# Optimization experiments

Measured on AMD Instinct MI355X. Metric: run time of the kernel, lower is better.

The kernel has to match this reference:

```python
import jax, jax.numpy as jnp
import numpy as np

B, CIN, CINT, H, W = 2, 2048, 512, 96, 96
CQK = CINT // 8  # 64, mmcv CrissCrossAttention query/key channels
NG = 32          # GroupNorm groups
EPS = 1e-5


def conv1x1(x, w, b):
    # x: [B,C,H,W], w: [O,C,1,1], b: [O]
    y = jnp.einsum('bchw,oc->bohw', x, w[:, :, 0, 0])
    return y + b[None, :, None, None]


def conv3x3(x, w):
    return jax.lax.conv_general_dilated(
        x, w, window_strides=(1, 1), padding=((1, 1), (1, 1)),
        dimension_numbers=('NCHW', 'OIHW', 'NCHW'))


def group_norm(x, gamma, beta):
    b, c, h, w = x.shape
    xg = x.reshape(b, NG, c // NG, h, w)
    mu = xg.mean(axis=(2, 3, 4), keepdims=True)
    var = xg.var(axis=(2, 3, 4), keepdims=True)
    xg = (xg - mu) * jax.lax.rsqrt(var + EPS)
    return xg.reshape(b, c, h, w) * gamma[None, :, None, None] + beta[None, :, None, None]


def criss_cross_attention(x, qw, qb, kw, kb, vw, vb, gamma):
    # mmcv CrissCrossAttention: attention restricted to each pixel's row + column.
    b, c, h, w = x.shape
    q = conv1x1(x, qw, qb)  # [B,Cqk,H,W]
    k = conv1x1(x, kw, kb)  # [B,Cqk,H,W]
    v = conv1x1(x, vw, vb)  # [B,C,H,W]
    # column (H-direction) energy: e_H[b,h,w,i] = sum_c q[b,c,h,w] k[b,c,i,w]
    e_h = jnp.einsum('bchw,bciw->bhwi', q, k)
    diag = jnp.eye(h, dtype=bool)[:, None, :]  # mask i==h (self counted once, in W branch)
    e_h = jnp.where(diag, -jnp.inf, e_h)
    # row (W-direction) energy: e_W[b,h,w,j] = sum_c q[b,c,h,w] k[b,c,h,j]
    e_w = jnp.einsum('bchw,bchj->bhwj', q, k)
    attn = jax.nn.softmax(jnp.concatenate([e_h, e_w], axis=-1), axis=-1)  # [B,H,W,H+W]
    a_h, a_w = attn[..., :h], attn[..., h:]
    out = jnp.einsum('bciw,bhwi->bchw', v, a_h) + jnp.einsum('bchj,bhwj->bchw', v, a_w)
    return gamma * out + x


def setup_inputs() -> dict:
    key = jax.random.key(0)
    ks = jax.random.split(key, 12)
    s = 0.02
    return {
        'x': jax.random.normal(ks[0], (B, CIN, H, W), jnp.float32),
        'conv1_w': jax.random.normal(ks[1], (CINT, CIN, 1, 1), jnp.float32) * s,
        'conv1_b': jnp.zeros((CINT,), jnp.float32),
        'q_w': jax.random.normal(ks[2], (CQK, CINT, 1, 1), jnp.float32) * s,
        'q_b': jnp.zeros((CQK,), jnp.float32),
        'k_w': jax.random.normal(ks[3], (CQK, CINT, 1, 1), jnp.float32) * s,
        'k_b': jnp.zeros((CQK,), jnp.float32),
        'v_w': jax.random.normal(ks[4], (CINT, CINT, 1, 1), jnp.float32) * s,
        'v_b': jnp.zeros((CINT,), jnp.float32),
        'gamma': jnp.asarray(0.5, jnp.float32),
        'convout_w': jax.random.normal(ks[5], (CINT, CINT, 3, 3), jnp.float32) * s,
        'gn_gamma': jnp.ones((CINT,), jnp.float32),
        'gn_beta': jnp.zeros((CINT,), jnp.float32),
    }


def reference(x, conv1_w, conv1_b, q_w, q_b, k_w, k_b, v_w, v_b, gamma,
              convout_w, gn_gamma, gn_beta):
    out = conv1x1(x, conv1_w, conv1_b)
    for _ in range(2):  # recurrence = 2
        out = criss_cross_attention(out, q_w, q_b, k_w, k_b, v_w, v_b, gamma)
    out = conv3x3(out, convout_w)  # ConvModule with GN => conv has no bias
    out = group_norm(out, gn_gamma, gn_beta)
    return out
```

## Files before the change

kernel.cpp:

```cpp
#include <hip/hip_runtime.h>
#include <hip/hip_bf16.h>


typedef __bf16 bf8_t __attribute__((ext_vector_type(8)));
typedef float f32x4 __attribute__((ext_vector_type(4)));

union I4B8 { int4 i; bf8_t b; };

typedef const __attribute__((address_space(1))) void as1_cvoid;
typedef __attribute__((address_space(3))) void as3_void;
__device__ __forceinline__ void gload16(const void* g, void* l) {
  __builtin_amdgcn_global_load_lds((as1_cvoid*)g, (as3_void*)l, 16, 0, 0);
}
__device__ __forceinline__ int rot8(int c, int key) { return (c + key) & 7; }

__global__ __launch_bounds__(256) void cast_rot_k(const float* s, __bf16* d, int K8, int total8) {
  int idx = blockIdx.x * 256 + threadIdx.x;
  if (idx >= total8) return;
  int c8 = idx % K8, n = idx / K8;
  int cch = c8 & 7;
  int pos = rot8(cch, n & 7);
  const float* sp = s + ((long long)n * K8 + c8) * 8;
  float4 a = *(const float4*)sp, b = *(const float4*)(sp + 4);
  I4B8 u;
  u.b[0] = (__bf16)a.x; u.b[1] = (__bf16)a.y; u.b[2] = (__bf16)a.z; u.b[3] = (__bf16)a.w;
  u.b[4] = (__bf16)b.x; u.b[5] = (__bf16)b.y; u.b[6] = (__bf16)b.z; u.b[7] = (__bf16)b.w;
  *(int4*)(d + ((long long)n * K8 + (c8 & ~7) + pos) * 8) = u.i;
}

__global__ __launch_bounds__(256) void wqkv_rot_k(const float* qw, const float* kw, const float* vw, __bf16* d) {
  int idx = blockIdx.x * 256 + threadIdx.x;
  if (idx >= 640 * 64) return;
  int c8 = idx & 63, n = idx >> 6;
  const float* src = (n < 64) ? qw + (long long)n * 512
                   : (n < 128) ? kw + (long long)(n - 64) * 512
                               : vw + (long long)(n - 128) * 512;
  int cch = c8 & 7;
  int pos = rot8(cch, n & 7);
  const float* sp = src + c8 * 8;
  float4 a = *(const float4*)sp, b = *(const float4*)(sp + 4);
  I4B8 u;
  u.b[0] = (__bf16)a.x; u.b[1] = (__bf16)a.y; u.b[2] = (__bf16)a.z; u.b[3] = (__bf16)a.w;
  u.b[4] = (__bf16)b.x; u.b[5] = (__bf16)b.y; u.b[6] = (__bf16)b.z; u.b[7] = (__bf16)b.w;
  *(int4*)(d + ((long long)n * 64 + (c8 & ~7) + pos) * 8) = u.i;
}

__global__ __launch_bounds__(256) void fuse_bias_k(const float* qb, const float* kb, const float* vb, float* d) {
  int i = blockIdx.x * 256 + threadIdx.x;
  if (i >= 640) return;
  d[i] = (i < 64) ? qb[i] : (i < 128) ? kb[i - 64] : vb[i - 128];
}

__global__ __launch_bounds__(256) void reorder_w_k(const float* w, __bf16* wr) {
  int idx = blockIdx.x * 256 + threadIdx.x;
  if (idx >= 512 * 9 * 64) return;
  int ch8 = idx & 63;
  int r = idx >> 6;
  int dydx = r % 9, o = r / 9;
  int k = dydx * 512 + ch8 * 8;
  int cch = (k >> 3) & 7;
  int pos = rot8(cch, o & 7);
  const float* src = w + ((long long)o * 512 + ch8 * 8) * 9 + dydx;
  I4B8 u;
#pragma unroll
  for (int j = 0; j < 8; j++) u.b[j] = (__bf16)src[j * 9];
  *(int4*)(wr + (long long)o * 4608 + (k & ~63) + pos * 8) = u.i;
}

__global__ __launch_bounds__(256) void transpose_x_k(const float* x, __bf16* xt) {
  __shared__ __bf16 l[64 * 66];
  int c0 = blockIdx.x * 64, s0 = blockIdx.y * 64, b = blockIdx.z;
  int t = threadIdx.x;
#pragma unroll
  for (int i = 0; i < 2; i++) {
    int slot = t + i * 256;
    int cl = slot >> 3, sch = slot & 7;
    const float* src = x + ((long long)(b * 2048 + c0 + cl)) * 9216 + s0 + sch * 8;
    float4 a = *(const float4*)src, bb = *(const float4*)(src + 4);
    __bf16* dst = &l[cl * 66 + sch * 8];
    dst[0] = (__bf16)a.x; dst[1] = (__bf16)a.y; dst[2] = (__bf16)a.z; dst[3] = (__bf16)a.w;
    dst[4] = (__bf16)bb.x; dst[5] = (__bf16)bb.y; dst[6] = (__bf16)bb.z; dst[7] = (__bf16)bb.w;
  }
  __syncthreads();
#pragma unroll
  for (int i = 0; i < 2; i++) {
    int slot = t + i * 256;
    int sl = slot >> 3, cch = slot & 7;
    I4B8 u;
#pragma unroll
    for (int j = 0; j < 8; j++) u.b[j] = l[(cch * 8 + j) * 66 + sl];
    *(int4*)(xt + ((long long)(b * 9216 + s0 + sl)) * 2048 + c0 + rot8(cch, sl & 7) * 8) = u.i;
  }
}

__global__ __launch_bounds__(256) void pad_k(const __bf16* y, __bf16* pout) {
  long long idx = (long long)blockIdx.x * 256 + threadIdx.x;
  int cch = (int)(idx & 63);
  long long r = idx >> 6;
  int ww = (int)(r % 98);
  long long r2 = r / 98;
  int hh = (int)(r2 % 98);
  int b = (int)(r2 / 98);
  int slice = cch >> 3, sub = cch & 7;
  int4 v = make_int4(0, 0, 0, 0);
  if (hh >= 1 && hh <= 96 && ww >= 1 && ww <= 96) {
    long long pix = (long long)b * 9216 + (hh - 1) * 96 + (ww - 1);
    v = *(const int4*)(y + pix * 512 + (slice * 8 + rot8(sub, (int)(pix & 7))) * 8);
  }
  *(int4*)(pout + r * 512 + (slice * 8 + rot8(sub, ww & 7)) * 8) = v;
}

struct GemmAP {
  const __bf16 *A, *B;
  __bf16* C;
  const float* bias;
  long long sAr, sBr, sCr;
  int K, ntn;
};

template <int CROT>
__global__ __launch_bounds__(256) void gemm_async_k(GemmAP p) {
  __shared__ __attribute__((aligned(16))) __bf16 lA[128 * 64];
  __shared__ __attribute__((aligned(16))) __bf16 lB[128 * 64];
  const int t = threadIdx.x;
  const int id = blockIdx.x;
  const int per8 = gridDim.x >> 3;
  const int lin = (id & 7) * per8 + (id >> 3);
  const int m0 = (lin / p.ntn) * 128, n0 = (lin % p.ntn) * 128;
  const int lane = t & 63, wave = t >> 6;
  const int wm = (wave >> 1) * 64, wn = (wave & 1) * 64;
  const int l15 = lane & 15, l4 = lane >> 4;
  const int srow = (lane >> 3), schunk = (lane & 7) * 8;
  f32x4 acc[4][4];
#pragma unroll
  for (int i = 0; i < 4; i++)
#pragma unroll
    for (int j = 0; j < 4; j++) acc[i][j] = f32x4{0.f, 0.f, 0.f, 0.f};

  for (int kb = 0; kb < p.K; kb += 64) {
    const int rb = wave * 32;
#pragma unroll
    for (int i = 0; i < 4; i++) {
      int row = rb + i * 8;
      gload16(p.A + (long long)(m0 + row + srow) * p.sAr + kb + schunk, &lA[row * 64]);
      gload16(p.B + (long long)(n0 + row + srow) * p.sBr + kb + schunk, &lB[row * 64]);
    }
    __syncthreads();
#pragma unroll
    for (int kk = 0; kk < 2; kk++) {
      bf8_t af[4], bfr[4];
      int cch = kk * 4 + l4;
#pragma unroll
      for (int mt = 0; mt < 4; mt++) {
        int r = wm + mt * 16 + l15;
        af[mt] = *(bf8_t*)&lA[r * 64 + (rot8(cch, r & 7) << 3)];
      }
#pragma unroll
      for (int nt = 0; nt < 4; nt++) {
        int r = wn + nt * 16 + l15;
        bfr[nt] = *(bf8_t*)&lB[r * 64 + (rot8(cch, r & 7) << 3)];
      }
#pragma unroll
      for (int mt = 0; mt < 4; mt++)
#pragma unroll
        for (int nt = 0; nt < 4; nt++)
          acc[mt][nt] = __builtin_amdgcn_mfma_f32_16x16x32_bf16(af[mt], bfr[nt], acc[mt][nt], 0, 0, 0);
    }
    __syncthreads();
  }
#pragma unroll
  for (int nt = 0; nt < 4; nt++) {
    int col = n0 + wn + nt * 16 + l15;
    float bv = p.bias[col];
#pragma unroll
    for (int mt = 0; mt < 4; mt++) {
      int row0 = m0 + wm + mt * 16 + (l4 << 2);
#pragma unroll
      for (int r = 0; r < 4; r++) {
        int row = row0 + r;
        int pc = CROT ? (col & ~63) + (rot8((col >> 3) & 7, row & 7) << 3) + (col & 7) : col;
        p.C[(long long)row * p.sCr + pc] = (__bf16)(acc[mt][nt][r] + bv);
      }
    }
  }
}

struct GemmP {
  const __bf16 *A, *B;
  __bf16* C;
  long long sAr, sAb1, sAb2;
  long long sBr, sBb1, sBb2;
  long long sCr, sCb1, sCb2;
  int M, N, K, bdiv, mode;
  const __bf16 *tmp, *res;
  const float* gma;
};

template <int CROT>
__global__ __launch_bounds__(256) void gemm_bt_k(GemmP p) {
  __shared__ __attribute__((aligned(16))) __bf16 lA[128 * 64];
  __shared__ __attribute__((aligned(16))) __bf16 lB[128 * 64];
  const int t = threadIdx.x;
  const int z = blockIdx.z;
  const int z1 = z / p.bdiv, z2 = z % p.bdiv;
  const __bf16* A = p.A + (long long)z1 * p.sAb1 + (long long)z2 * p.sAb2;
  const __bf16* B = p.B + (long long)z1 * p.sBb1 + (long long)z2 * p.sBb2;
  const int m0 = blockIdx.y * 128, n0 = blockIdx.x * 128;
  const int lane = t & 63, wave = t >> 6;
  const int wm = (wave >> 1) * 64, wn = (wave & 1) * 64;
  const int l15 = lane & 15, l4 = lane >> 4;
  f32x4 acc[4][4];
#pragma unroll
  for (int i = 0; i < 4; i++)
#pragma unroll
    for (int j = 0; j < 4; j++) acc[i][j] = f32x4{0.f, 0.f, 0.f, 0.f};

  int arow[4];
#pragma unroll
  for (int i = 0; i < 4; i++) {
    int slot = t + i * 256;
    arow[i] = min(m0 + (slot >> 3), p.M - 1);
  }
  for (int kb = 0; kb < p.K; kb += 64) {
#pragma unroll
    for (int i = 0; i < 4; i++) {
      int slot = t + i * 256;
      int r = slot >> 3, c = slot & 7;
      int gk = kb + c * 8;
      int4 v = make_int4(0, 0, 0, 0);
      if (gk < p.K) v = *(const int4*)(A + (long long)arow[i] * p.sAr + gk);
      *(int4*)&lA[r * 64 + (rot8(c, r & 7) << 3)] = v;
    }
#pragma unroll
    for (int i = 0; i < 4; i++) {
      int slot = t + i * 256;
      int kl = slot & 63, cch = slot >> 6;
      int gk = kb + kl;
      I4B8 u;
      u.i = make_int4(0, 0, 0, 0);
      if (gk < p.K) u.i = *(const int4*)(B + (long long)gk * p.sBr + n0 + cch * 8);
#pragma unroll
      for (int j = 0; j < 8; j++) {
        int n = cch * 8 + j;
        lB[n * 64 + (rot8(kl >> 3, n & 7) << 3) + (kl & 7)] = u.b[j];
      }
    }
    __syncthreads();
#pragma unroll
    for (int kk = 0; kk < 2; kk++) {
      bf8_t af[4], bfr[4];
      int cch = kk * 4 + l4;
#pragma unroll
      for (int mt = 0; mt < 4; mt++) {
        int r = wm + mt * 16 + l15;
        af[mt] = *(bf8_t*)&lA[r * 64 + (rot8(cch, r & 7) << 3)];
      }
#pragma unroll
      for (int nt = 0; nt < 4; nt++) {
        int r = wn + nt * 16 + l15;
        bfr[nt] = *(bf8_t*)&lB[r * 64 + (rot8(cch, r & 7) << 3)];
      }
#pragma unroll
      for (int mt = 0; mt < 4; mt++)
#pragma unroll
        for (int nt = 0; nt < 4; nt++)
          acc[mt][nt] = __builtin_amdgcn_mfma_f32_16x16x32_bf16(af[mt], bfr[nt], acc[mt][nt], 0, 0, 0);
    }
    __syncthreads();
  }
  long long coff = (long long)z1 * p.sCb1 + (long long)z2 * p.sCb2;
  float g = (p.mode == 2) ? *p.gma : 0.f;
#pragma unroll
  for (int nt = 0; nt < 4; nt++) {
    int col = n0 + wn + nt * 16 + l15;
    if (col >= p.N) continue;
#pragma unroll
    for (int mt = 0; mt < 4; mt++) {
      int row0 = m0 + wm + mt * 16 + (l4 << 2);
#pragma unroll
      for (int r = 0; r < 4; r++) {
        int row = row0 + r;
        if (row >= p.M) continue;
        long long offL = coff + (long long)row * p.sCr + col;
        long long offP = offL;
        if (CROT)
          offP = coff + (long long)row * p.sCr +
                 (col & ~63) + (rot8((col >> 3) & 7, row & 7) << 3) + (col & 7);
        float v = acc[mt][nt][r];
        if (p.mode == 2)
          v = g * ((float)p.tmp[offL] + v) + (float)p.res[offP];
        p.C[offP] = (__bf16)v;
      }
    }
  }
}

__global__ __launch_bounds__(384) void cc_scores_k(const __bf16* qkv, float* attnf) {
  __shared__ __attribute__((aligned(16))) __bf16 Qs[96 * 64];
  __shared__ __attribute__((aligned(16))) __bf16 Ks[96 * 64];
  int bfi = blockIdx.x;
  int b = bfi / 96, f = bfi % 96;
  int mode = blockIdx.y;
  long long base = (mode == 0) ? ((long long)(b * 9216 + f)) * 640 : ((long long)(b * 9216 + f * 96)) * 640;
  long long rstr = (mode == 0) ? 96 * 640 : 640;
  int t = threadIdx.x;
#pragma unroll
  for (int i = 0; i < 2; i++) {
    int slot = t + i * 384;
    int r = slot >> 3, c = slot & 7;
    int sw = rot8(c, r & 7) << 3;
    *(int4*)&Qs[r * 64 + sw] = *(const int4*)(qkv + base + (long long)r * rstr + c * 8);
    *(int4*)&Ks[r * 64 + sw] = *(const int4*)(qkv + base + (long long)r * rstr + 64 + c * 8);
  }
  __syncthreads();
  int lane = t & 63, wave = t >> 6;
  int l15 = lane & 15, l4 = lane >> 4;
  f32x4 acc[6];
#pragma unroll
  for (int i = 0; i < 6; i++) acc[i] = f32x4{0.f, 0.f, 0.f, 0.f};
#pragma unroll
  for (int kk = 0; kk < 2; kk++) {
    int ar = wave * 16 + l15;
    int cch = kk * 4 + l4;
    bf8_t af = *(bf8_t*)&Qs[ar * 64 + (rot8(cch, ar & 7) << 3)];
#pragma unroll
    for (int nt = 0; nt < 6; nt++) {
      int br = nt * 16 + l15;
      bf8_t bfr = *(bf8_t*)&Ks[br * 64 + (rot8(cch, br & 7) << 3)];
      acc[nt] = __builtin_amdgcn_mfma_f32_16x16x32_bf16(af, bfr, acc[nt], 0, 0, 0);
    }
  }
#pragma unroll
  for (int nt = 0; nt < 6; nt++) {
#pragma unroll
    for (int r = 0; r < 4; r++) {
      int m = wave * 16 + (l4 << 2) + r;
      int n = nt * 16 + l15;
      float v = acc[nt][r];
      long long off;
      if (mode == 0) {
        if (n == m) v = -__builtin_inff();
        off = ((long long)((b * 96 + m) * 96 + f)) * 192 + n;
      } else {
        off = ((long long)((b * 96 + f) * 96 + m)) * 192 + 96 + n;
      }
      attnf[off] = v;
    }
  }
}

__global__ __launch_bounds__(256) void cc_softmax_k(const float* attnf, __bf16* attnb) {
  int wave = threadIdx.x >> 6, lane = threadIdx.x & 63;
  long long row = (long long)blockIdx.x * 4 + wave;
  const float* src = attnf + row * 192;
  float e0 = src[lane], e1 = src[lane + 64], e2 = src[lane + 128];
  float m = fmaxf(e0, fmaxf(e1, e2));
#pragma unroll
  for (int o = 32; o; o >>= 1) m = fmaxf(m, __shfl_xor(m, o));
  e0 = __expf(e0 - m);
  e1 = __expf(e1 - m);
  e2 = __expf(e2 - m);
  float s = e0 + e1 + e2;
#pragma unroll
  for (int o = 32; o; o >>= 1) s += __shfl_xor(s, o);
  float inv = 1.f / s;
  __bf16* dst = attnb + row * 192;
  dst[lane] = (__bf16)(e0 * inv);
  dst[lane + 64] = (__bf16)(e1 * inv);
  dst[lane + 128] = (__bf16)(e2 * inv);
}

__global__ __launch_bounds__(256) void conv3_gemm_k(const __bf16* pin, const __bf16* wr, __bf16* C) {
  __shared__ __attribute__((aligned(16))) __bf16 lA[128 * 64];
  __shared__ __attribute__((aligned(16))) __bf16 lB[128 * 64];
  const int t = threadIdx.x;
  const int id = blockIdx.x;
  const int per8 = gridDim.x >> 3;
  const int lin = (id & 7) * per8 + (id >> 3);
  const int m0 = (lin >> 2) * 128, n0 = (lin & 3) * 128;
  const int lane = t & 63, wave = t >> 6;
  const int wm = (wave >> 1) * 64, wn = (wave & 1) * 64;
  const int l15 = lane & 15, l4 = lane >> 4;
  const int srow = lane >> 3, schunk = (lane & 7) * 8;
  const int rb = wave * 32;
  f32x4 acc[4][4];
#pragma unroll
  for (int i = 0; i < 4; i++)
#pragma unroll
    for (int j = 0; j < 4; j++) acc[i][j] = f32x4{0.f, 0.f, 0.f, 0.f};
  long long sbase[4], bbase[4];
#pragma unroll
  for (int i = 0; i < 4; i++) {
    int r = rb + i * 8 + srow;
    int m = m0 + r;
    int b = m / 9216, hw = m % 9216;
    int h = hw / 96, w2 = hw % 96;
    sbase[i] = ((long long)b * 9604 + h * 98 + w2) * 512 + schunk;
    bbase[i] = (long long)(n0 + r) * 4608 + schunk;
  }
  int w2f[4];
#pragma unroll
  for (int mt = 0; mt < 4; mt++) w2f[mt] = (m0 + wm + mt * 16 + l15) % 96;

  int kt = 0;
  for (int tap = 0; tap < 9; tap++) {
    const int dy = tap / 3, dx = tap - dy * 3;
    const long long aoff = (long long)(dy * 98 + dx) * 512;
    int keyA[4];
#pragma unroll
    for (int mt = 0; mt < 4; mt++) keyA[mt] = (w2f[mt] + dx) & 7;
    for (int sl = 0; sl < 8; sl++, kt++) {
      const int c0k = sl * 64;
#pragma unroll
      for (int i = 0; i < 4; i++) {
        gload16(pin + sbase[i] + aoff + c0k, &lA[(rb + i * 8) * 64]);
        gload16(wr + bbase[i] + kt * 64, &lB[(rb + i * 8) * 64]);
      }
      __syncthreads();
#pragma unroll
      for (int kk = 0; kk < 2; kk++) {
        bf8_t af[4], bfr[4];
        int cch = kk * 4 + l4;
#pragma unroll
        for (int mt = 0; mt < 4; mt++) {
          int r = wm + mt * 16 + l15;
          af[mt] = *(bf8_t*)&lA[r * 64 + (rot8(cch, keyA[mt]) << 3)];
        }
#pragma unroll
        for (int nt = 0; nt < 4; nt++) {
          int r = wn + nt * 16 + l15;
          bfr[nt] = *(bf8_t*)&lB[r * 64 + (rot8(cch, r & 7) << 3)];
        }
#pragma unroll
        for (int mt = 0; mt < 4; mt++)
#pragma unroll
          for (int nt = 0; nt < 4; nt++)
            acc[mt][nt] = __builtin_amdgcn_mfma_f32_16x16x32_bf16(af[mt], bfr[nt], acc[mt][nt], 0, 0, 0);
      }
      __syncthreads();
    }
  }
#pragma unroll
  for (int nt = 0; nt < 4; nt++) {
    int col = n0 + wn + nt * 16 + l15;
#pragma unroll
    for (int mt = 0; mt < 4; mt++) {
      int row0 = m0 + wm + mt * 16 + (l4 << 2);
#pragma unroll
      for (int r = 0; r < 4; r++) {
        int row = row0 + r;
        C[(long long)row * 512 + col] = (__bf16)acc[mt][nt][r];
      }
    }
  }
}

__global__ __launch_bounds__(256) void gn_stats_k(const __bf16* z, float* stats) {
  int bg = blockIdx.x;
  int b = bg >> 5, g = bg & 31;
  int t = threadIdx.x;
  int cch = t & 1, sp0 = t >> 1;
  const __bf16* base = z + (long long)b * 9216 * 512 + g * 16 + cch * 8;
  float s = 0.f, ss = 0.f;
  for (int sp = sp0; sp < 9216; sp += 128) {
    I4B8 u;
    u.i = *(const int4*)(base + (long long)sp * 512);
#pragma unroll
    for (int j = 0; j < 8; j++) {
      float f = (float)u.b[j];
      s += f;
      ss += f * f;
    }
  }
#pragma unroll
  for (int o = 32; o; o >>= 1) {
    s += __shfl_xor(s, o);
    ss += __shfl_xor(ss, o);
  }
  __shared__ float red[8];
  int wave = t >> 6, lane = t & 63;
  if (lane == 0) {
    red[wave] = s;
    red[4 + wave] = ss;
  }
  __syncthreads();
  if (t == 0) {
    float S = red[0] + red[1] + red[2] + red[3];
    float SS = red[4] + red[5] + red[6] + red[7];
    const float inv = 1.f / 147456.f;
    float mean = S * inv;
    float var = SS * inv - mean * mean;
    stats[2 * bg] = mean;
    stats[2 * bg + 1] = rsqrtf(var + 1e-5f);
  }
}

__global__ __launch_bounds__(256) void gn_write_k(const __bf16* z, const float* stats,
                                                 const float* gng, const float* gnb, float* out) {
  __shared__ __bf16 l[64 * 98];
  int c0 = blockIdx.x * 64, h = blockIdx.y, b = blockIdx.z;
  int t = threadIdx.x;
#pragma unroll
  for (int i = 0; i < 3; i++) {
    int slot = t + i * 256;
    int wl = slot >> 3, cch = slot & 7;
    I4B8 u;
    u.i = *(const int4*)(z + ((long long)(b * 9216 + h * 96 + wl)) * 512 + c0 + cch * 8);
#pragma unroll
    for (int j = 0; j < 8; j++) l[(cch * 8 + j) * 98 + wl] = u.b[j];
  }
  __syncthreads();
#pragma unroll
  for (int i = 0; i < 3; i++) {
    int slot = t + i * 256;
    int wch = slot % 12, cl = slot / 12;
    int c = c0 + cl;
    int g = c >> 4;
    float mean = stats[2 * (b * 32 + g)], rstd = stats[2 * (b * 32 + g) + 1];
    float sc = rstd * gng[c];
    float sh = gnb[c] - mean * sc;
    float4 o0, o1;
    const __bf16* src = &l[cl * 98 + wch * 8];
    o0.x = (float)src[0] * sc + sh; o0.y = (float)src[1] * sc + sh;
    o0.z = (float)src[2] * sc + sh; o0.w = (float)src[3] * sc + sh;
    o1.x = (float)src[4] * sc + sh; o1.y = (float)src[5] * sc + sh;
    o1.z = (float)src[6] * sc + sh; o1.w = (float)src[7] * sc + sh;
    float* dst = out + ((long long)((b * 512 + c) * 96 + h)) * 96 + wch * 8;
    *(float4*)dst = o0;
    *(float4*)(dst + 4) = o1;
  }
}

extern "C" void kernel_launch(void* const* d_in, const int* in_sizes, int n_in,
                              void* d_out, int out_size, void* d_ws, size_t ws_size,
                              hipStream_t stream) {
  (void)in_sizes; (void)n_in; (void)out_size;
  const float* x = (const float*)d_in[0];
  const float* conv1w = (const float*)d_in[1];
  const float* conv1b = (const float*)d_in[2];
  const float* qw = (const float*)d_in[3];
  const float* qbias = (const float*)d_in[4];
  const float* kw = (const float*)d_in[5];
  const float* kbias = (const float*)d_in[6];
  const float* vw = (const float*)d_in[7];
  const float* vbias = (const float*)d_in[8];
  const float* gma = (const float*)d_in[9];
  const float* cow = (const float*)d_in[10];
  const float* gng = (const float*)d_in[11];
  const float* gnb = (const float*)d_in[12];
  float* out = (float*)d_out;

  if (ws_size < 134876160ULL) return;

  char* w = (char*)d_ws;
  __bf16* xt    = (__bf16*)(w);
  __bf16* qkv   = (__bf16*)(w);
  __bf16* attnb = (__bf16*)(w + 23592960);
  __bf16* padb  = (__bf16*)(w);
  __bf16* zb    = (__bf16*)(w + 19668992);
  __bf16* wrot  = (__bf16*)(w + 38543360);
  __bf16* ya    = (__bf16*)(w + 75497472);
  __bf16* yb    = (__bf16*)(w + 94371840);
  __bf16* tmp1  = (__bf16*)(w + 113246208);
  float* attnf  = (float*)(w + 113246208);
  __bf16* c1wb  = (__bf16*)(w + 132120576);
  __bf16* wqkvb = (__bf16*)(w + 134217728);
  float* qkvbias = (float*)(w + 134873088);
  float* stats   = (float*)(w + 134875648);

  cast_rot_k<<<512, 256, 0, stream>>>(conv1w, c1wb, 256, 131072);
  wqkv_rot_k<<<160, 256, 0, stream>>>(qw, kw, vw, wqkvb);
  fuse_bias_k<<<3, 256, 0, stream>>>(qbias, kbias, vbias, qkvbias);
  transpose_x_k<<<dim3(32, 144, 2), 256, 0, stream>>>(x, xt);

  {
    GemmAP p{};
    p.A = xt; p.B = c1wb; p.C = ya; p.bias = conv1b;
    p.sAr = 2048; p.sBr = 2048; p.sCr = 512;
    p.K = 2048; p.ntn = 4;
    gemm_async_k<1><<<576, 256, 0, stream>>>(p);
  }

  for (int it = 0; it < 2; it++) {
    __bf16* tin = it ? yb : ya;
    __bf16* tout = it ? ya : yb;
    {
      GemmAP p{};
      p.A = tin; p.B = wqkvb; p.C = qkv; p.bias = qkvbias;
      p.sAr = 512; p.sBr = 512; p.sCr = 640;
      p.K = 512; p.ntn = 5;
      gemm_async_k<0><<<720, 256, 0, stream>>>(p);
    }
    cc_scores_k<<<dim3(192, 2), 384, 0, stream>>>(qkv, attnf);
    cc_softmax_k<<<4608, 256, 0, stream>>>(attnf, attnb);
    {
      GemmP p{};
      p.A = attnb; p.sAr = 96 * 192; p.sAb1 = (long long)96 * 96 * 192; p.sAb2 = 192;
      p.B = qkv + 128; p.sBr = (long long)96 * 640; p.sBb1 = (long long)9216 * 640; p.sBb2 = 640;
      p.C = tmp1; p.sCr = (long long)96 * 512; p.sCb1 = (long long)9216 * 512; p.sCb2 = 512;
      p.M = 96; p.N = 512; p.K = 96; p.bdiv = 96; p.mode = 0;
      gemm_bt_k<0><<<dim3(4, 1, 192), 256, 0, stream>>>(p);
    }
    {
      GemmP p{};
      p.A = attnb + 96; p.sAr = 192; p.sAb1 = (long long)96 * 96 * 192; p.sAb2 = (long long)96 * 192;
      p.B = qkv + 128; p.sBr = 640; p.sBb1 = (long long)9216 * 640; p.sBb2 = (long long)96 * 640;
      p.C = tout; p.sCr = 512; p.sCb1 = (long long)9216 * 512; p.sCb2 = (long long)96 * 512;
      p.M = 96; p.N = 512; p.K = 96; p.bdiv = 96; p.mode = 2;
      p.tmp = tmp1; p.res = tin; p.gma = gma;
      gemm_bt_k<1><<<dim3(4, 1, 192), 256, 0, stream>>>(p);
    }
  }

  reorder_w_k<<<1152, 256, 0, stream>>>(cow, wrot);
  pad_k<<<4802, 256, 0, stream>>>(ya, padb);
  conv3_gemm_k<<<576, 256, 0, stream>>>(padb, wrot, zb);
  gn_stats_k<<<64, 256, 0, stream>>>(zb, stats);
  gn_write_k<<<dim3(8, 96, 2), 256, 0, stream>>>(zb, stats, gng, gnb, out);
}
```

Before: 693.1 us.

## Split attention buffers, fuse padding into aggregation epilogue, async-load attention tiles

Scores are written in contiguous per-column and per-row blocks, and softmax emits separate swizzled, K-padded H and W attention matrices. The aggregation GEMMs can then load A tiles with async global-to-LDS loads and a fixed K of 128. The final aggregation writes straight into the padded conv input, so the pad kernel becomes a border-zeroing kernel. The weight reorder now stages through LDS for coalesced reads. The cost is a more complex softmax store pattern and an extra workspace layout.

```diff
diff --git a/kernel.cpp b/kernel.cpp
--- a/kernel.cpp
+++ b/kernel.cpp
@@ -18,8 +18,7 @@
   int idx = blockIdx.x * 256 + threadIdx.x;
   if (idx >= total8) return;
   int c8 = idx % K8, n = idx / K8;
-  int cch = c8 & 7;
-  int pos = rot8(cch, n & 7);
+  int pos = rot8(c8 & 7, n & 7);
   const float* sp = s + ((long long)n * K8 + c8) * 8;
   float4 a = *(const float4*)sp, b = *(const float4*)(sp + 4);
   I4B8 u;
@@ -35,8 +34,7 @@
   const float* src = (n < 64) ? qw + (long long)n * 512
                    : (n < 128) ? kw + (long long)(n - 64) * 512
                                : vw + (long long)(n - 128) * 512;
-  int cch = c8 & 7;
-  int pos = rot8(cch, n & 7);
+  int pos = rot8(c8 & 7, n & 7);
   const float* sp = src + c8 * 8;
   float4 a = *(const float4*)sp, b = *(const float4*)(sp + 4);
   I4B8 u;
@@ -52,19 +50,25 @@
 }
 
 __global__ __launch_bounds__(256) void reorder_w_k(const float* w, __bf16* wr) {
-  int idx = blockIdx.x * 256 + threadIdx.x;
-  if (idx >= 512 * 9 * 64) return;
-  int ch8 = idx & 63;
-  int r = idx >> 6;
-  int dydx = r % 9, o = r / 9;
-  int k = dydx * 512 + ch8 * 8;
-  int cch = (k >> 3) & 7;
-  int pos = rot8(cch, o & 7);
-  const float* src = w + ((long long)o * 512 + ch8 * 8) * 9 + dydx;
-  I4B8 u;
-#pragma unroll
-  for (int j = 0; j < 8; j++) u.b[j] = (__bf16)src[j * 9];
-  *(int4*)(wr + (long long)o * 4608 + (k & ~63) + pos * 8) = u.i;
+  __shared__ float ls[4608];
+  int o = blockIdx.x;
+  int t = threadIdx.x;
+  const float* base = w + (long long)o * 4608;
+#pragma unroll
+  for (int i = 0; i < 18; i++) ls[t + i * 256] = base[t + i * 256];
+  __syncthreads();
+#pragma unroll
+  for (int i = 0; i < 3; i++) {
+    int q = t + i * 256;
+    if (q >= 576) break;
+    int k0 = q * 8;
+    int dydx = k0 / 512, c0 = k0 & 511;
+    I4B8 u;
+#pragma unroll
+    for (int j = 0; j < 8; j++) u.b[j] = (__bf16)ls[(c0 + j) * 9 + dydx];
+    int pos = rot8((k0 >> 3) & 7, o & 7);
+    *(int4*)(wr + (long long)o * 4608 + (k0 & ~63) + pos * 8) = u.i;
+  }
 }
 
 __global__ __launch_bounds__(256) void transpose_x_k(const float* x, __bf16* xt) {
@@ -93,21 +97,17 @@
   }
 }
 
-__global__ __launch_bounds__(256) void pad_k(const __bf16* y, __bf16* pout) {
-  long long idx = (long long)blockIdx.x * 256 + threadIdx.x;
-  int cch = (int)(idx & 63);
-  long long r = idx >> 6;
-  int ww = (int)(r % 98);
-  long long r2 = r / 98;
-  int hh = (int)(r2 % 98);
-  int b = (int)(r2 / 98);
-  int slice = cch >> 3, sub = cch & 7;
-  int4 v = make_int4(0, 0, 0, 0);
-  if (hh >= 1 && hh <= 96 && ww >= 1 && ww <= 96) {
-    long long pix = (long long)b * 9216 + (hh - 1) * 96 + (ww - 1);
-    v = *(const int4*)(y + pix * 512 + (slice * 8 + rot8(sub, (int)(pix & 7))) * 8);
-  }
-  *(int4*)(pout + r * 512 + (slice * 8 + rot8(sub, ww & 7)) * 8) = v;
+__global__ __launch_bounds__(256) void border0_k(__bf16* padb) {
+  int idx = blockIdx.x * 256 + threadIdx.x;
+  if (idx >= 776 * 64) return;
+  int ch = idx & 63, bi = idx >> 6;
+  int b = bi / 388, r = bi % 388;
+  int hh, ww;
+  if (r < 98) { hh = 0; ww = r; }
+  else if (r < 196) { hh = 97; ww = r - 98; }
+  else if (r < 292) { hh = r - 196 + 1; ww = 0; }
+  else { hh = r - 292 + 1; ww = 97; }
+  *(int4*)(padb + ((long long)(b * 9604 + hh * 98 + ww)) * 512 + ch * 8) = make_int4(0, 0, 0, 0);
 }
 
 struct GemmAP {
@@ -185,51 +185,42 @@
   }
 }
 
-struct GemmP {
+struct AggP {
   const __bf16 *A, *B;
   __bf16* C;
-  long long sAr, sAb1, sAb2;
-  long long sBr, sBb1, sBb2;
-  long long sCr, sCb1, sCb2;
-  int M, N, K, bdiv, mode;
   const __bf16 *tmp, *res;
   const float* gma;
+  long long bB1, bB2, sBr;
+  long long cB1, cB2, sCr;
 };
 
-template <int CROT>
-__global__ __launch_bounds__(256) void gemm_bt_k(GemmP p) {
+template <int MODE>
+__global__ __launch_bounds__(256) void agg_k(AggP p) {
   __shared__ __attribute__((aligned(16))) __bf16 lA[128 * 64];
   __shared__ __attribute__((aligned(16))) __bf16 lB[128 * 64];
   const int t = threadIdx.x;
   const int z = blockIdx.z;
-  const int z1 = z / p.bdiv, z2 = z % p.bdiv;
-  const __bf16* A = p.A + (long long)z1 * p.sAb1 + (long long)z2 * p.sAb2;
-  const __bf16* B = p.B + (long long)z1 * p.sBb1 + (long long)z2 * p.sBb2;
-  const int m0 = blockIdx.y * 128, n0 = blockIdx.x * 128;
+  const int z1 = z / 96, z2 = z % 96;
+  const __bf16* A = p.A + (long long)z * (96 * 128);
+  const __bf16* B = p.B + (long long)z1 * p.bB1 + (long long)z2 * p.bB2;
+  const int n0 = blockIdx.x * 128;
   const int lane = t & 63, wave = t >> 6;
   const int wm = (wave >> 1) * 64, wn = (wave & 1) * 64;
   const int l15 = lane & 15, l4 = lane >> 4;
+  const int srow = lane >> 3, schunk = (lane & 7) * 8;
   f32x4 acc[4][4];
 #pragma unroll
   for (int i = 0; i < 4; i++)
 #pragma unroll
     for (int j = 0; j < 4; j++) acc[i][j] = f32x4{0.f, 0.f, 0.f, 0.f};
 
-  int arow[4];
-#pragma unroll
-  for (int i = 0; i < 4; i++) {
-    int slot = t + i * 256;
-    arow[i] = min(m0 + (slot >> 3), p.M - 1);
-  }
-  for (int kb = 0; kb < p.K; kb += 64) {
+#pragma unroll
+  for (int kb = 0; kb < 128; kb += 64) {
+    const int rb = wave * 32;
 #pragma unroll
     for (int i = 0; i < 4; i++) {
-      int slot = t + i * 256;
-      int r = slot >> 3, c = slot & 7;
-      int gk = kb + c * 8;
-      int4 v = make_int4(0, 0, 0, 0);
-      if (gk < p.K) v = *(const int4*)(A + (long long)arow[i] * p.sAr + gk);
-      *(int4*)&lA[r * 64 + (rot8(c, r & 7) << 3)] = v;
+      int row = rb + i * 8;
+      gload16(A + (long long)(row + srow) * 128 + kb + schunk, &lA[row * 64]);
     }
 #pragma unroll
     for (int i = 0; i < 4; i++) {
@@ -238,7 +229,7 @@
       int gk = kb + kl;
       I4B8 u;
       u.i = make_int4(0, 0, 0, 0);
-      if (gk < p.K) u.i = *(const int4*)(B + (long long)gk * p.sBr + n0 + cch * 8);
+      if (gk < 96) u.i = *(const int4*)(B + (long long)gk * p.sBr + n0 + cch * 8);
 #pragma unroll
       for (int j = 0; j < 8; j++) {
         int n = cch * 8 + j;
@@ -268,34 +259,40 @@
     }
     __syncthreads();
   }
-  long long coff = (long long)z1 * p.sCb1 + (long long)z2 * p.sCb2;
-  float g = (p.mode == 2) ? *p.gma : 0.f;
+  long long cbase = (long long)z1 * p.cB1 + (long long)z2 * p.cB2;
+  float g = MODE ? *p.gma : 0.f;
 #pragma unroll
   for (int nt = 0; nt < 4; nt++) {
     int col = n0 + wn + nt * 16 + l15;
-    if (col >= p.N) continue;
 #pragma unroll
     for (int mt = 0; mt < 4; mt++) {
-      int row0 = m0 + wm + mt * 16 + (l4 << 2);
+      int row0 = wm + mt * 16 + (l4 << 2);
 #pragma unroll
       for (int r = 0; r < 4; r++) {
         int row = row0 + r;
-        if (row >= p.M) continue;
-        long long offL = coff + (long long)row * p.sCr + col;
-        long long offP = offL;
-        if (CROT)
-          offP = coff + (long long)row * p.sCr +
-                 (col & ~63) + (rot8((col >> 3) & 7, row & 7) << 3) + (col & 7);
+        if (row >= 96) continue;
+        long long offL = cbase + (long long)row * p.sCr + col;
         float v = acc[mt][nt][r];
-        if (p.mode == 2)
+        if (MODE == 0) {
+          p.C[offL] = (__bf16)v;
+        } else {
+          int rc = (col & ~63) + (rot8((col >> 3) & 7, row & 7) << 3) + (col & 7);
+          long long offP = cbase + (long long)row * p.sCr + rc;
           v = g * ((float)p.tmp[offL] + v) + (float)p.res[offP];
-        p.C[offP] = (__bf16)v;
-      }
-    }
-  }
-}
-
-__global__ __launch_bounds__(384) void cc_scores_k(const __bf16* qkv, float* attnf) {
+          if (MODE == 1) {
+            p.C[offP] = (__bf16)v;
+          } else {
+            int pc = (col & ~63) + (rot8((col >> 3) & 7, (row + 1) & 7) << 3) + (col & 7);
+            long long pidx = (long long)z1 * 9604 + (long long)(z2 + 1) * 98 + (row + 1);
+            p.C[pidx * 512 + pc] = (__bf16)v;
+          }
+        }
+      }
+    }
+  }
+}
+
+__global__ __launch_bounds__(384) void cc_scores_k(const __bf16* qkv, float* attnfH, float* attnfW) {
   __shared__ __attribute__((aligned(16))) __bf16 Qs[96 * 64];
   __shared__ __attribute__((aligned(16))) __bf16 Ks[96 * 64];
   int bfi = blockIdx.x;
@@ -330,6 +327,7 @@
       acc[nt] = __builtin_amdgcn_mfma_f32_16x16x32_bf16(af, bfr, acc[nt], 0, 0, 0);
     }
   }
+  float* dst = (mode == 0 ? attnfH : attnfW) + (long long)bfi * 9216;
 #pragma unroll
   for (int nt = 0; nt < 6; nt++) {
 #pragma unroll
@@ -337,37 +335,44 @@
       int m = wave * 16 + (l4 << 2) + r;
       int n = nt * 16 + l15;
       float v = acc[nt][r];
-      long long off;
-      if (mode == 0) {
-        if (n == m) v = -__builtin_inff();
-        off = ((long long)((b * 96 + m) * 96 + f)) * 192 + n;
-      } else {
-        off = ((long long)((b * 96 + f) * 96 + m)) * 192 + 96 + n;
-      }
-      attnf[off] = v;
-    }
-  }
-}
-
-__global__ __launch_bounds__(256) void cc_softmax_k(const float* attnf, __bf16* attnb) {
+      if (mode == 0 && n == m) v = -__builtin_inff();
+      dst[m * 96 + n] = v;
+    }
+  }
+}
+
+__global__ __launch_bounds__(256) void cc_softmax_k(const float* attnfH, const float* attnfW,
+                                                    __bf16* a_h, __bf16* a_w) {
   int wave = threadIdx.x >> 6, lane = threadIdx.x & 63;
-  long long row = (long long)blockIdx.x * 4 + wave;
-  const float* src = attnf + row * 192;
-  float e0 = src[lane], e1 = src[lane + 64], e2 = src[lane + 128];
-  float m = fmaxf(e0, fmaxf(e1, e2));
+  int pix = blockIdx.x * 4 + wave;
+  int b = pix / 9216, hw = pix % 9216;
+  int h = hw / 96, w2 = hw % 96;
+  const float* ehb = attnfH + ((long long)(b * 96 + w2)) * 9216 + h * 96;
+  const float* ewb = attnfW + ((long long)(b * 96 + h)) * 9216 + w2 * 96;
+  float x0 = ehb[lane];
+  float x1 = lane < 32 ? ehb[64 + lane] : -__builtin_inff();
+  float x2 = ewb[lane];
+  float x3 = lane < 32 ? ewb[64 + lane] : -__builtin_inff();
+  float m = fmaxf(fmaxf(x0, x1), fmaxf(x2, x3));
 #pragma unroll
   for (int o = 32; o; o >>= 1) m = fmaxf(m, __shfl_xor(m, o));
-  e0 = __expf(e0 - m);
-  e1 = __expf(e1 - m);
-  e2 = __expf(e2 - m);
-  float s = e0 + e1 + e2;
+  float e0 = __expf(x0 - m), e1 = __expf(x1 - m), e2 = __expf(x2 - m), e3 = __expf(x3 - m);
+  float s = e0 + e1 + e2 + e3;
 #pragma unroll
   for (int o = 32; o; o >>= 1) s += __shfl_xor(s, o);
   float inv = 1.f / s;
-  __bf16* dst = attnb + row * 192;
-  dst[lane] = (__bf16)(e0 * inv);
-  dst[lane + 64] = (__bf16)(e1 * inv);
-  dst[lane + 128] = (__bf16)(e2 * inv);
+  __bf16* dh = a_h + ((long long)((b * 96 + w2) * 96 + h)) * 128;
+  __bf16* dw = a_w + ((long long)((b * 96 + h) * 96 + w2)) * 128;
+  int kh = h & 7, kw2 = w2 & 7;
+  int k1 = lane, k2 = 64 + lane;
+  int p1h = (k1 & ~63) + (rot8((k1 >> 3) & 7, kh) << 3) + (k1 & 7);
+  int p2h = (k2 & ~63) + (rot8((k2 >> 3) & 7, kh) << 3) + (k2 & 7);
+  int p1w = (k1 & ~63) + (rot8((k1 >> 3) & 7, kw2) << 3) + (k1 & 7);
+  int p2w = (k2 & ~63) + (rot8((k2 >> 3) & 7, kw2) << 3) + (k2 & 7);
+  dh[p1h] = (__bf16)(e0 * inv);
+  dh[p2h] = (__bf16)(lane < 32 ? e1 * inv : 0.f);
+  dw[p1w] = (__bf16)(e2 * inv);
+  dw[p2w] = (__bf16)(lane < 32 ? e3 * inv : 0.f);
 }
 
 __global__ __launch_bounds__(256) void conv3_gemm_k(const __bf16* pin, const __bf16* wr, __bf16* C) {
@@ -553,18 +558,20 @@
   if (ws_size < 134876160ULL) return;
 
   char* w = (char*)d_ws;
-  __bf16* xt    = (__bf16*)(w);
-  __bf16* qkv   = (__bf16*)(w);
-  __bf16* attnb = (__bf16*)(w + 23592960);
-  __bf16* padb  = (__bf16*)(w);
-  __bf16* zb    = (__bf16*)(w + 19668992);
-  __bf16* wrot  = (__bf16*)(w + 38543360);
-  __bf16* ya    = (__bf16*)(w + 75497472);
-  __bf16* yb    = (__bf16*)(w + 94371840);
-  __bf16* tmp1  = (__bf16*)(w + 113246208);
-  float* attnf  = (float*)(w + 113246208);
-  __bf16* c1wb  = (__bf16*)(w + 132120576);
-  __bf16* wqkvb = (__bf16*)(w + 134217728);
+  __bf16* xt     = (__bf16*)(w);
+  __bf16* qkv    = (__bf16*)(w);
+  float* attnfH  = (float*)(w + 23592960);
+  float* attnfW  = (float*)(w + 30670848);
+  __bf16* a_h    = (__bf16*)(w + 37748736);
+  __bf16* a_w    = (__bf16*)(w + 42467328);
+  __bf16* padb   = (__bf16*)(w + 47185920);
+  __bf16* wrot   = (__bf16*)(w + 66854912);
+  __bf16* ya     = (__bf16*)(w + 75497472);
+  __bf16* yb     = (__bf16*)(w + 94371840);
+  __bf16* tmp1   = (__bf16*)(w + 113246208);
+  __bf16* zb     = (__bf16*)(w);
+  __bf16* c1wb   = (__bf16*)(w + 132120576);
+  __bf16* wqkvb  = (__bf16*)(w + 134217728);
   float* qkvbias = (float*)(w + 134873088);
   float* stats   = (float*)(w + 134875648);
 
@@ -583,7 +590,6 @@
 
   for (int it = 0; it < 2; it++) {
     __bf16* tin = it ? yb : ya;
-    __bf16* tout = it ? ya : yb;
     {
       GemmAP p{};
       p.A = tin; p.B = wqkvb; p.C = qkv; p.bias = qkvbias;
@@ -591,29 +597,33 @@
       p.K = 512; p.ntn = 5;
       gemm_async_k<0><<<720, 256, 0, stream>>>(p);
     }
-    cc_scores_k<<<dim3(192, 2), 384, 0, stream>>>(qkv, attnf);
-    cc_softmax_k<<<4608, 256, 0, stream>>>(attnf, attnb);
+    cc_scores_k<<<dim3(192, 2), 384, 0, stream>>>(qkv, attnfH, attnfW);
+    cc_softmax_k<<<4608, 256, 0, stream>>>(attnfH, attnfW, a_h, a_w);
     {
-      GemmP p{};
-      p.A = attnb; p.sAr = 96 * 192; p.sAb1 = (long long)96 * 96 * 192; p.sAb2 = 192;
-      p.B = qkv + 128; p.sBr = (long long)96 * 640; p.sBb1 = (long long)9216 * 640; p.sBb2 = 640;
-      p.C = tmp1; p.sCr = (long long)96 * 512; p.sCb1 = (long long)9216 * 512; p.sCb2 = 512;
-      p.M = 96; p.N = 512; p.K = 96; p.bdiv = 96; p.mode = 0;
-      gemm_bt_k<0><<<dim3(4, 1, 192), 256, 0, stream>>>(p);
+      AggP p{};
+      p.A = a_h; p.B = qkv + 128; p.C = tmp1;
+      p.bB1 = (long long)9216 * 640; p.bB2 = 640; p.sBr = (long long)96 * 640;
+      p.cB1 = (long long)9216 * 512; p.cB2 = 512; p.sCr = (long long)96 * 512;
+      agg_k<0><<<dim3(4, 1, 192), 256, 0, stream>>>(p);
     }
     {
-      GemmP p{};
-      p.A = attnb + 96; p.sAr = 192; p.sAb1 = (long long)96 * 96 * 192; p.sAb2 = (long long)96 * 192;
-      p.B = qkv + 128; p.sBr = 640; p.sBb1 = (long long)9216 * 640; p.sBb2 = (long long)96 * 640;
-      p.C = tout; p.sCr = 512; p.sCb1 = (long long)9216 * 512; p.sCb2 = (long long)96 * 512;
-      p.M = 96; p.N = 512; p.K = 96; p.bdiv = 96; p.mode = 2;
+      AggP p{};
+      p.A = a_w; p.B = qkv + 128;
+      p.bB1 = (long long)9216 * 640; p.bB2 = (long long)96 * 640; p.sBr = 640;
+      p.cB1 = (long long)9216 * 512; p.cB2 = (long long)96 * 512; p.sCr = 512;
       p.tmp = tmp1; p.res = tin; p.gma = gma;
-      gemm_bt_k<1><<<dim3(4, 1, 192), 256, 0, stream>>>(p);
-    }
-  }
-
-  reorder_w_k<<<1152, 256, 0, stream>>>(cow, wrot);
-  pad_k<<<4802, 256, 0, stream>>>(ya, padb);
+      if (it == 0) {
+        p.C = yb;
+        agg_k<1><<<dim3(4, 1, 192), 256, 0, stream>>>(p);
+      } else {
+        p.C = padb;
+        agg_k<2><<<dim3(4, 1, 192), 256, 0, stream>>>(p);
+      }
+    }
+  }
+
+  reorder_w_k<<<512, 256, 0, stream>>>(cow, wrot);
+  border0_k<<<194, 256, 0, stream>>>(padb);
   conv3_gemm_k<<<576, 256, 0, stream>>>(padb, wrot, zb);
   gn_stats_k<<<64, 256, 0, stream>>>(zb, stats);
   gn_write_k<<<dim3(8, 96, 2), 256, 0, stream>>>(zb, stats, gng, gnb, out);
```

Result: faster. 660.9 us (-4.7%).
